# Kernel optimization log

Hardware: AMD Instinct MI355X
Metric: run time of the kernel (lower is better)

The kernel has to match this reference:

```python
import jax, jax.numpy as jnp
import numpy as np

N, C, H, W = 8, 256, 28, 28
K = 64
EPS = 1e-12  # F.normalize eps
BN_EPS = 1e-5


def setup_inputs() -> dict:
    key = jax.random.key(0)
    k1, k2, k3 = jax.random.split(key, 3)
    x = jax.random.normal(k1, (N, C, H, W), dtype=jnp.float32)
    conv_w = jax.random.normal(k2, (K, C), dtype=jnp.float32) * 0.05  # 1x1 conv, no bias (vlad_v2=False)
    centroids = jax.random.uniform(k3, (K, C), dtype=jnp.float32)    # torch.rand init
    bn_w = jnp.ones((K * C,), dtype=jnp.float32)
    bn_b = jnp.zeros((K * C,), dtype=jnp.float32)
    return {"x": x, "conv_w": conv_w, "centroids": centroids, "bn_w": bn_w, "bn_b": bn_b}


def _l2norm(v, axis):
    n = jnp.sqrt(jnp.sum(v * v, axis=axis, keepdims=True))
    return v / jnp.maximum(n, EPS)


def reference(x, conv_w, centroids, bn_w, bn_b):
    n, c, h, w = x.shape
    k = centroids.shape[0]
    P = h * w
    # descriptor-wise L2 normalize over channels
    xn = _l2norm(x, axis=1)
    xf = xn.reshape(n, c, P)                                   # (N, C, P)
    # 1x1 conv soft assignment + softmax over clusters
    soft_assign = jnp.einsum('ncp,kc->nkp', xf, conv_w)        # (N, K, P)
    soft_assign = jax.nn.softmax(soft_assign, axis=1)
    # weighted residuals (N, K, C, P)
    residual = (xf[:, None, :, :] - centroids[None, :, :, None]) * soft_assign[:, :, None, :]
    # intra-normalize over flattened (K*C) per spatial location
    rn = jnp.sqrt(jnp.sum(residual * residual, axis=(1, 2), keepdims=True))  # (N,1,1,P)
    residual = residual / jnp.maximum(rn, EPS)
    # sum pool over spatial, then per-cluster L2 normalize over C
    vlad = residual.sum(axis=-1)                               # (N, K, C)
    vlad = _l2norm(vlad, axis=2)
    v = vlad.reshape(n, k * c)
    # BatchNorm1d in training mode: batch stats, biased variance
    mean = jnp.mean(v, axis=0)
    var = jnp.var(v, axis=0)
    v = (v - mean) / jnp.sqrt(var + BN_EPS) * bn_w + bn_b
    # final L2 normalize
    return _l2norm(v, axis=1)
```

## Files before the change

kernel.cpp:

```cpp
#include <hip/hip_runtime.h>
#include <math.h>

#define N_ 8
#define C_ 256
#define P_ 784
#define K_ 64
#define NP_ 6272
#define F_ 16384
#define FEPS 1e-12f
#define BNEPS 1e-5f

__device__ __forceinline__ float wave_sum(float v) {
#pragma unroll
  for (int s = 1; s < 64; s <<= 1) v += __shfl_xor(v, s, 64);
  return v;
}
__device__ __forceinline__ float wave_max(float v) {
#pragma unroll
  for (int s = 1; s < 64; s <<= 1) v = fmaxf(v, __shfl_xor(v, s, 64));
  return v;
}

__global__ __launch_bounds__(256) void k_prep(const float* __restrict__ x,
                                              const float* __restrict__ cent,
                                              float* __restrict__ rinv,
                                              float* __restrict__ xn2,
                                              float* __restrict__ cn2) {
  __shared__ float red[4][64];
  int b = blockIdx.x, t = threadIdx.x;
  if (b < 25) {
    int tid = b * 256 + t;
    if (tid < NP_) {
      int n = tid / P_, p = tid % P_;
      const float* base = x + (size_t)n * C_ * P_ + p;
      float ssq = 0.f;
#pragma unroll 8
      for (int c = 0; c < C_; ++c) { float v = base[(size_t)c * P_]; ssq += v * v; }
      float r = 1.0f / fmaxf(sqrtf(ssq), FEPS);
      rinv[tid] = r;
      xn2[tid] = ssq * r * r;
    }
  } else {
    int k = t & 63, part = t >> 6;
    const float* row = cent + (size_t)k * C_ + part * 64;
    float s = 0.f;
#pragma unroll 8
    for (int i = 0; i < 64; ++i) { float v = row[i]; s += v * v; }
    red[part][k] = s;
    __syncthreads();
    if (t < 64) cn2[t] = red[0][t] + red[1][t] + red[2][t] + red[3][t];
  }
}

__global__ __launch_bounds__(256) void k_gemm1(const float* __restrict__ x,
                                               const float* __restrict__ convw,
                                               const float* __restrict__ cent,
                                               float* __restrict__ Gp) {
  __shared__ float AsT[32][68];
  __shared__ float Xs[32][68];
  int z = blockIdx.z;
  int n = z >> 1, half = z & 1;
  int kk0 = blockIdx.y * 64;
  int p0 = blockIdx.x * 64;
  int t = threadIdx.x;
  int tx = t & 15, ty = t >> 4;
  float acc[4][4] = {};
  const float* xb = x + (size_t)n * C_ * P_;
  int cbase = half * 128;
  for (int c0 = cbase; c0 < cbase + 128; c0 += 32) {
    {
      int r = t >> 5, cc = t & 31;
#pragma unroll
      for (int i = 0; i < 8; ++i) {
        int row = r + i * 8;
        int kk = kk0 + row;
        const float* Ar = (kk < 64) ? (convw + (size_t)kk * C_) : (cent + (size_t)(kk - 64) * C_);
        AsT[cc][row] = Ar[c0 + cc];
      }
    }
    {
      int rr = t >> 6, pp = t & 63;
#pragma unroll
      for (int i = 0; i < 8; ++i) {
        int c = rr + i * 4;
        int p = p0 + pp;
        Xs[c][pp] = (p < P_) ? xb[(size_t)(c0 + c) * P_ + p] : 0.f;
      }
    }
    __syncthreads();
#pragma unroll
    for (int cc = 0; cc < 32; ++cc) {
      float4 a = *(const float4*)&AsT[cc][ty * 4];
      float4 bv = *(const float4*)&Xs[cc][tx * 4];
      float av[4] = {a.x, a.y, a.z, a.w};
      float bb[4] = {bv.x, bv.y, bv.z, bv.w};
#pragma unroll
      for (int i = 0; i < 4; ++i)
#pragma unroll
        for (int j = 0; j < 4; ++j) acc[i][j] += av[i] * bb[j];
    }
    __syncthreads();
  }
  float* Gb = Gp + (size_t)(half * N_ + n) * P_ * 128;
#pragma unroll
  for (int j = 0; j < 4; ++j) {
    int p = p0 + tx * 4 + j;
    if (p < P_) {
      float4 v = make_float4(acc[0][j], acc[1][j], acc[2][j], acc[3][j]);
      *(float4*)&Gb[(size_t)p * 128 + kk0 + ty * 4] = v;
    }
  }
}

__global__ __launch_bounds__(256) void k_assign(const float* __restrict__ Gp,
                                                const float* __restrict__ rinv,
                                                const float* __restrict__ xn2v,
                                                const float* __restrict__ cn2,
                                                float* __restrict__ w2,
                                                float* __restrict__ Spart) {
  __shared__ float w2_lds[64][17];
  __shared__ float w_lds[64][17];
  int n = blockIdx.y;
  int p0 = blockIdx.x * 16;
  int t = threadIdx.x;
  int wv = t >> 6, lane = t & 63;
  float c2 = cn2[lane];
  const float* Gb0 = Gp + (size_t)n * P_ * 128;
  const float* Gb1 = Gp + (size_t)(N_ + n) * P_ * 128;
  for (int j = 0; j < 4; ++j) {
    int p = p0 + wv * 4 + j;
    float r = rinv[n * P_ + p];
    float lg = (Gb0[(size_t)p * 128 + lane] + Gb1[(size_t)p * 128 + lane]) * r;
    float dt = (Gb0[(size_t)p * 128 + 64 + lane] + Gb1[(size_t)p * 128 + 64 + lane]) * r;
    float m = wave_max(lg);
    float e = expf(lg - m);
    float ssum = wave_sum(e);
    float a = e / ssum;
    float x2 = xn2v[n * P_ + p];
    float rn2 = wave_sum(a * a * (x2 - 2.f * dt + c2));
    float wf = 1.0f / fmaxf(sqrtf(rn2), FEPS);
    float wval = a * wf;
    w_lds[lane][wv * 4 + j] = wval;
    w2_lds[lane][wv * 4 + j] = wval * r;
  }
  __syncthreads();
  {
    int pp = t & 15, k4 = t >> 4;
    float* wb = w2 + (size_t)n * K_ * P_ + p0 + pp;
#pragma unroll
    for (int i = 0; i < 4; ++i) {
      int k = k4 + i * 16;
      wb[(size_t)k * P_] = w2_lds[k][pp];
    }
  }
  if (t < 64) {
    float s = 0.f;
#pragma unroll
    for (int pp = 0; pp < 16; ++pp) s += w_lds[t][pp];
    Spart[((size_t)blockIdx.x * N_ + n) * 64 + t] = s;
  }
}

__global__ __launch_bounds__(256) void k_gemm2(const float* __restrict__ x,
                                               const float* __restrict__ w2,
                                               float* __restrict__ vpart) {
  __shared__ float WsT[32][68];
  __shared__ float XsT[32][68];
  int n = blockIdx.z, s = blockIdx.y;
  int c0 = blockIdx.x * 64;
  int t = threadIdx.x;
  int tx = t & 15, ty = t >> 4;
  float acc[4][4] = {};
  const float* wb = w2 + (size_t)n * K_ * P_;
  const float* xb = x + (size_t)n * C_ * P_;
  int pbase = s * 98;
  for (int q = 0; q < 98; q += 32) {
    int r = t >> 5, pc = t & 31;
    bool ok = (q + pc) < 98;
    int p = pbase + q + pc;
#pragma unroll
    for (int i = 0; i < 8; ++i) {
      int row = r + i * 8;
      WsT[pc][row] = ok ? wb[(size_t)row * P_ + p] : 0.f;
      XsT[pc][row] = ok ? xb[(size_t)(c0 + row) * P_ + p] : 0.f;
    }
    __syncthreads();
#pragma unroll
    for (int pp = 0; pp < 32; ++pp) {
      float4 a = *(const float4*)&WsT[pp][ty * 4];
      float4 bv = *(const float4*)&XsT[pp][tx * 4];
      float av[4] = {a.x, a.y, a.z, a.w};
      float bb[4] = {bv.x, bv.y, bv.z, bv.w};
#pragma unroll
      for (int i = 0; i < 4; ++i)
#pragma unroll
        for (int j = 0; j < 4; ++j) acc[i][j] += av[i] * bb[j];
    }
    __syncthreads();
  }
  float* vb = vpart + (size_t)(s * N_ + n) * K_ * C_;
#pragma unroll
  for (int i = 0; i < 4; ++i)
#pragma unroll
    for (int j = 0; j < 4; ++j)
      vb[(size_t)(ty * 4 + i) * C_ + c0 + tx * 4 + j] = acc[i][j];
}

__global__ __launch_bounds__(256) void k_vladnorm(const float* __restrict__ vpart,
                                                  const float* __restrict__ cent,
                                                  const float* __restrict__ Spart,
                                                  float* __restrict__ vladn) {
  __shared__ float red[4];
  int b = blockIdx.x;
  int n = b >> 6, k = b & 63;
  int c = threadIdx.x;
  float Sb = 0.f;
#pragma unroll
  for (int s = 0; s < 49; ++s) Sb += Spart[((size_t)s * N_ + n) * 64 + k];
  float val = 0.f;
#pragma unroll
  for (int s = 0; s < 8; ++s) val += vpart[(size_t)(s * 512 + b) * C_ + c];
  val -= cent[(size_t)k * C_ + c] * Sb;
  float ss = wave_sum(val * val);
  int wv = threadIdx.x >> 6, lane = threadIdx.x & 63;
  if (lane == 0) red[wv] = ss;
  __syncthreads();
  float tot = red[0] + red[1] + red[2] + red[3];
  float inv = 1.0f / fmaxf(sqrtf(tot), FEPS);
  vladn[(size_t)b * C_ + c] = val * inv;
}

__global__ __launch_bounds__(256) void k_bn(const float* __restrict__ vladn,
                                            const float* __restrict__ bnw,
                                            const float* __restrict__ bnb,
                                            float* __restrict__ ybuf,
                                            float* __restrict__ nrmpart) {
  __shared__ float red[4][8];
  int f = blockIdx.x * 256 + threadIdx.x;
  float v[N_];
  float s = 0.f;
#pragma unroll
  for (int n = 0; n < N_; ++n) { v[n] = vladn[(size_t)n * F_ + f]; s += v[n]; }
  float mean = s * (1.0f / N_);
  float s2 = 0.f;
#pragma unroll
  for (int n = 0; n < N_; ++n) { float d = v[n] - mean; s2 += d * d; }
  float var = s2 * (1.0f / N_);
  float sc = bnw[f] / sqrtf(var + BNEPS);
  float bb = bnb[f];
  float y[N_];
#pragma unroll
  for (int n = 0; n < N_; ++n) {
    y[n] = (v[n] - mean) * sc + bb;
    ybuf[(size_t)n * F_ + f] = y[n];
  }
  int wv = threadIdx.x >> 6, lane = threadIdx.x & 63;
#pragma unroll
  for (int n = 0; n < N_; ++n) {
    float q = wave_sum(y[n] * y[n]);
    if (lane == 0) red[wv][n] = q;
  }
  __syncthreads();
  if (threadIdx.x < N_) {
    int n = threadIdx.x;
    nrmpart[n * 64 + blockIdx.x] = red[0][n] + red[1][n] + red[2][n] + red[3][n];
  }
}

__global__ __launch_bounds__(256) void k_final(const float* __restrict__ ybuf,
                                               const float* __restrict__ nrmpart,
                                               float* __restrict__ out) {
  int idx = blockIdx.x * 256 + threadIdx.x;
  int n = idx >> 14;
  float tot = 0.f;
#pragma unroll
  for (int b = 0; b < 64; ++b) tot += nrmpart[n * 64 + b];
  float inv = 1.0f / fmaxf(sqrtf(tot), FEPS);
  out[idx] = ybuf[idx] * inv;
}

extern "C" void kernel_launch(void* const* d_in, const int* in_sizes, int n_in,
                              void* d_out, int out_size, void* d_ws, size_t ws_size,
                              hipStream_t stream) {
  const float* x = (const float*)d_in[0];
  const float* convw = (const float*)d_in[1];
  const float* cent = (const float*)d_in[2];
  const float* bnw = (const float*)d_in[3];
  const float* bnb = (const float*)d_in[4];
  float* out = (float*)d_out;
  float* ws = (float*)d_ws;

  float* rinv = ws;
  float* xn2 = ws + 6272;
  float* cn2 = ws + 12544;
  float* Spart = ws + 12608;
  float* nrmpart = ws + 37696;
  float* Gp = ws + 38208;
  float* w2 = ws + 1643840;
  float* vpart = ws + 2045248;
  float* vladn = ws + 3093824;
  float* ybuf = ws + 3224896;

  k_prep<<<26, 256, 0, stream>>>(x, cent, rinv, xn2, cn2);
  k_gemm1<<<dim3(13, 2, 16), 256, 0, stream>>>(x, convw, cent, Gp);
  k_assign<<<dim3(49, 8), 256, 0, stream>>>(Gp, rinv, xn2, cn2, w2, Spart);
  k_gemm2<<<dim3(4, 8, 8), 256, 0, stream>>>(x, w2, vpart);
  k_vladnorm<<<512, 256, 0, stream>>>(vpart, cent, Spart, vladn);
  k_bn<<<64, 256, 0, stream>>>(vladn, bnw, bnb, ybuf, nrmpart);
  k_final<<<512, 256, 0, stream>>>(ybuf, nrmpart, out);
}
```

Before: 68.26 us.

## Fuse prep, assignment GEMM and softmax assign into a single kernel

Replaces the separate k_prep, k_gemm1 and k_assign kernels with one k_fused1 kernel. Each block owns 32 spatial positions of one image. It computes the full-channel logits and centroid dot products, the descriptor norms and the centroid norms in LDS, then does softmax and intra-normalization in place. This removes two kernel launches and the global round trip of the split-K GEMM partials. The cost is fewer blocks (200) with less parallel work per launch, and the Spart partial count drops from 49 to 25.

```diff
diff --git a/kernel.cpp b/kernel.cpp
--- a/kernel.cpp
+++ b/kernel.cpp
@@ -5,10 +5,10 @@
 #define C_ 256
 #define P_ 784
 #define K_ 64
-#define NP_ 6272
 #define F_ 16384
 #define FEPS 1e-12f
 #define BNEPS 1e-5f
+#define PBLK 25
 
 __device__ __forceinline__ float wave_sum(float v) {
 #pragma unroll
@@ -21,143 +21,137 @@
   return v;
 }
 
-__global__ __launch_bounds__(256) void k_prep(const float* __restrict__ x,
-                                              const float* __restrict__ cent,
-                                              float* __restrict__ rinv,
-                                              float* __restrict__ xn2,
-                                              float* __restrict__ cn2) {
-  __shared__ float red[4][64];
-  int b = blockIdx.x, t = threadIdx.x;
-  if (b < 25) {
-    int tid = b * 256 + t;
-    if (tid < NP_) {
-      int n = tid / P_, p = tid % P_;
-      const float* base = x + (size_t)n * C_ * P_ + p;
-      float ssq = 0.f;
-#pragma unroll 8
-      for (int c = 0; c < C_; ++c) { float v = base[(size_t)c * P_]; ssq += v * v; }
-      float r = 1.0f / fmaxf(sqrtf(ssq), FEPS);
-      rinv[tid] = r;
-      xn2[tid] = ssq * r * r;
-    }
-  } else {
-    int k = t & 63, part = t >> 6;
-    const float* row = cent + (size_t)k * C_ + part * 64;
-    float s = 0.f;
-#pragma unroll 8
-    for (int i = 0; i < 64; ++i) { float v = row[i]; s += v * v; }
-    red[part][k] = s;
-    __syncthreads();
-    if (t < 64) cn2[t] = red[0][t] + red[1][t] + red[2][t] + red[3][t];
-  }
-}
-
-__global__ __launch_bounds__(256) void k_gemm1(const float* __restrict__ x,
-                                               const float* __restrict__ convw,
-                                               const float* __restrict__ cent,
-                                               float* __restrict__ Gp) {
-  __shared__ float AsT[32][68];
-  __shared__ float Xs[32][68];
-  int z = blockIdx.z;
-  int n = z >> 1, half = z & 1;
-  int kk0 = blockIdx.y * 64;
-  int p0 = blockIdx.x * 64;
-  int t = threadIdx.x;
-  int tx = t & 15, ty = t >> 4;
-  float acc[4][4] = {};
-  const float* xb = x + (size_t)n * C_ * P_;
-  int cbase = half * 128;
-  for (int c0 = cbase; c0 < cbase + 128; c0 += 32) {
-    {
-      int r = t >> 5, cc = t & 31;
-#pragma unroll
-      for (int i = 0; i < 8; ++i) {
-        int row = r + i * 8;
-        int kk = kk0 + row;
-        const float* Ar = (kk < 64) ? (convw + (size_t)kk * C_) : (cent + (size_t)(kk - 64) * C_);
-        AsT[cc][row] = Ar[c0 + cc];
-      }
-    }
-    {
-      int rr = t >> 6, pp = t & 63;
-#pragma unroll
-      for (int i = 0; i < 8; ++i) {
-        int c = rr + i * 4;
-        int p = p0 + pp;
-        Xs[c][pp] = (p < P_) ? xb[(size_t)(c0 + c) * P_ + p] : 0.f;
-      }
-    }
-    __syncthreads();
-#pragma unroll
-    for (int cc = 0; cc < 32; ++cc) {
-      float4 a = *(const float4*)&AsT[cc][ty * 4];
-      float4 bv = *(const float4*)&Xs[cc][tx * 4];
-      float av[4] = {a.x, a.y, a.z, a.w};
-      float bb[4] = {bv.x, bv.y, bv.z, bv.w};
-#pragma unroll
-      for (int i = 0; i < 4; ++i)
-#pragma unroll
-        for (int j = 0; j < 4; ++j) acc[i][j] += av[i] * bb[j];
-    }
-    __syncthreads();
-  }
-  float* Gb = Gp + (size_t)(half * N_ + n) * P_ * 128;
-#pragma unroll
-  for (int j = 0; j < 4; ++j) {
-    int p = p0 + tx * 4 + j;
-    if (p < P_) {
-      float4 v = make_float4(acc[0][j], acc[1][j], acc[2][j], acc[3][j]);
-      *(float4*)&Gb[(size_t)p * 128 + kk0 + ty * 4] = v;
-    }
-  }
-}
-
-__global__ __launch_bounds__(256) void k_assign(const float* __restrict__ Gp,
-                                                const float* __restrict__ rinv,
-                                                const float* __restrict__ xn2v,
-                                                const float* __restrict__ cn2,
+__global__ __launch_bounds__(256) void k_fused1(const float* __restrict__ x,
+                                                const float* __restrict__ convw,
+                                                const float* __restrict__ cent,
                                                 float* __restrict__ w2,
                                                 float* __restrict__ Spart) {
-  __shared__ float w2_lds[64][17];
-  __shared__ float w_lds[64][17];
-  int n = blockIdx.y;
-  int p0 = blockIdx.x * 16;
+  __shared__ float As[128][33];
+  __shared__ float Xs[32][36];
+  __shared__ float G_lds[128][33];
+  __shared__ float w2_lds[64][33];
+  __shared__ float ssq_lds[8][32];
+  __shared__ float cn2p[256];
+  __shared__ float cn2_lds[64];
+  __shared__ float rinv_lds[32];
+  __shared__ float xn2_lds[32];
+  __shared__ float sp_lds[4][64];
+
+  int pblk = blockIdx.x, n = blockIdx.y;
+  int p0 = pblk * 32;
   int t = threadIdx.x;
   int wv = t >> 6, lane = t & 63;
-  float c2 = cn2[lane];
-  const float* Gb0 = Gp + (size_t)n * P_ * 128;
-  const float* Gb1 = Gp + (size_t)(N_ + n) * P_ * 128;
-  for (int j = 0; j < 4; ++j) {
-    int p = p0 + wv * 4 + j;
-    float r = rinv[n * P_ + p];
-    float lg = (Gb0[(size_t)p * 128 + lane] + Gb1[(size_t)p * 128 + lane]) * r;
-    float dt = (Gb0[(size_t)p * 128 + 64 + lane] + Gb1[(size_t)p * 128 + 64 + lane]) * r;
+  const float* xb = x + (size_t)n * C_ * P_;
+
+  {
+    int k = t >> 2, q = t & 3;
+    const float* row = cent + (size_t)k * C_ + q * 64;
+    float s = 0.f;
+#pragma unroll
+    for (int i = 0; i < 16; ++i) {
+      float4 v = *(const float4*)&row[i * 4];
+      s += v.x * v.x + v.y * v.y + v.z * v.z + v.w * v.w;
+    }
+    cn2p[t] = s;
+  }
+
+  int ty = t >> 3, tx = t & 7;
+  float acc[4][4] = {};
+  float ssq_reg = 0.f;
+
+  for (int ch = 0; ch < 8; ++ch) {
+    int c0 = ch * 32;
+    {
+      int cc = t & 31, kg = t >> 5;
+#pragma unroll
+      for (int i = 0; i < 16; ++i) {
+        int kk = kg * 16 + i;
+        const float* Ar = (kk < 64) ? (convw + (size_t)kk * C_) : (cent + (size_t)(kk - 64) * C_);
+        As[kk][cc] = Ar[c0 + cc];
+      }
+    }
+    {
+      int pp = t & 31, cg = t >> 5;
+      int p = p0 + pp;
+      bool ok = p < P_;
+#pragma unroll
+      for (int i = 0; i < 4; ++i) {
+        int cl = cg * 4 + i;
+        float v = ok ? xb[(size_t)(c0 + cl) * P_ + p] : 0.f;
+        Xs[cl][pp] = v;
+        ssq_reg += v * v;
+      }
+    }
+    __syncthreads();
+    if (ch == 0 && t < 64)
+      cn2_lds[t] = cn2p[t * 4] + cn2p[t * 4 + 1] + cn2p[t * 4 + 2] + cn2p[t * 4 + 3];
+#pragma unroll
+    for (int cc = 0; cc < 32; ++cc) {
+      float4 xv = *(const float4*)&Xs[cc][tx * 4];
+      float xa[4] = {xv.x, xv.y, xv.z, xv.w};
+#pragma unroll
+      for (int i = 0; i < 4; ++i) {
+        float a = As[ty * 4 + i][cc];
+#pragma unroll
+        for (int j = 0; j < 4; ++j) acc[i][j] += a * xa[j];
+      }
+    }
+    __syncthreads();
+  }
+
+#pragma unroll
+  for (int i = 0; i < 4; ++i)
+#pragma unroll
+    for (int j = 0; j < 4; ++j) G_lds[ty * 4 + i][tx * 4 + j] = acc[i][j];
+  ssq_lds[t >> 5][t & 31] = ssq_reg;
+  __syncthreads();
+  if (t < 32) {
+    float s = 0.f;
+#pragma unroll
+    for (int g = 0; g < 8; ++g) s += ssq_lds[g][t];
+    float r = 1.0f / fmaxf(sqrtf(s), FEPS);
+    rinv_lds[t] = r;
+    xn2_lds[t] = s * r * r;
+  }
+  __syncthreads();
+
+  float s_acc = 0.f;
+  float c2 = cn2_lds[lane];
+  for (int jp = 0; jp < 8; ++jp) {
+    int pl = wv * 8 + jp;
+    if (p0 + pl >= P_) break;
+    float r = rinv_lds[pl];
+    float x2 = xn2_lds[pl];
+    float lg = G_lds[lane][pl] * r;
+    float dt = G_lds[64 + lane][pl] * r;
     float m = wave_max(lg);
     float e = expf(lg - m);
     float ssum = wave_sum(e);
     float a = e / ssum;
-    float x2 = xn2v[n * P_ + p];
     float rn2 = wave_sum(a * a * (x2 - 2.f * dt + c2));
     float wf = 1.0f / fmaxf(sqrtf(rn2), FEPS);
     float wval = a * wf;
-    w_lds[lane][wv * 4 + j] = wval;
-    w2_lds[lane][wv * 4 + j] = wval * r;
-  }
-  __syncthreads();
+    s_acc += wval;
+    w2_lds[lane][pl] = wval * r;
+  }
+  sp_lds[wv][lane] = s_acc;
+  __syncthreads();
+  if (t < 64) {
+    float s = sp_lds[0][t] + sp_lds[1][t] + sp_lds[2][t] + sp_lds[3][t];
+    Spart[((size_t)pblk * N_ + n) * 64 + t] = s;
+  }
   {
-    int pp = t & 15, k4 = t >> 4;
-    float* wb = w2 + (size_t)n * K_ * P_ + p0 + pp;
-#pragma unroll
-    for (int i = 0; i < 4; ++i) {
-      int k = k4 + i * 16;
-      wb[(size_t)k * P_] = w2_lds[k][pp];
-    }
-  }
-  if (t < 64) {
-    float s = 0.f;
-#pragma unroll
-    for (int pp = 0; pp < 16; ++pp) s += w_lds[t][pp];
-    Spart[((size_t)blockIdx.x * N_ + n) * 64 + t] = s;
+    int q = t & 7;
+#pragma unroll
+    for (int it = 0; it < 2; ++it) {
+      int k = (t >> 3) + 32 * it;
+      int pidx = q * 4;
+      if (p0 + pidx + 3 < P_) {
+        float4 v = make_float4(w2_lds[k][pidx], w2_lds[k][pidx + 1],
+                               w2_lds[k][pidx + 2], w2_lds[k][pidx + 3]);
+        *(float4*)&w2[((size_t)n * K_ + k) * P_ + p0 + pidx] = v;
+      }
+    }
   }
 }
 
@@ -216,7 +210,7 @@
   int c = threadIdx.x;
   float Sb = 0.f;
 #pragma unroll
-  for (int s = 0; s < 49; ++s) Sb += Spart[((size_t)s * N_ + n) * 64 + k];
+  for (int s = 0; s < PBLK; ++s) Sb += Spart[((size_t)s * N_ + n) * 64 + k];
   float val = 0.f;
 #pragma unroll
   for (int s = 0; s < 8; ++s) val += vpart[(size_t)(s * 512 + b) * C_ + c];
@@ -290,20 +284,14 @@
   float* out = (float*)d_out;
   float* ws = (float*)d_ws;
 
-  float* rinv = ws;
-  float* xn2 = ws + 6272;
-  float* cn2 = ws + 12544;
-  float* Spart = ws + 12608;
-  float* nrmpart = ws + 37696;
-  float* Gp = ws + 38208;
-  float* w2 = ws + 1643840;
-  float* vpart = ws + 2045248;
-  float* vladn = ws + 3093824;
-  float* ybuf = ws + 3224896;
-
-  k_prep<<<26, 256, 0, stream>>>(x, cent, rinv, xn2, cn2);
-  k_gemm1<<<dim3(13, 2, 16), 256, 0, stream>>>(x, convw, cent, Gp);
-  k_assign<<<dim3(49, 8), 256, 0, stream>>>(Gp, rinv, xn2, cn2, w2, Spart);
+  float* Spart = ws;
+  float* nrmpart = ws + 12800;
+  float* w2 = ws + 13312;
+  float* vpart = ws + 414720;
+  float* vladn = ws + 1463296;
+  float* ybuf = ws + 1594368;
+
+  k_fused1<<<dim3(PBLK, N_), 256, 0, stream>>>(x, convw, cent, w2, Spart);
   k_gemm2<<<dim3(4, 8, 8), 256, 0, stream>>>(x, w2, vpart);
   k_vladnorm<<<512, 256, 0, stream>>>(vpart, cent, Spart, vladn);
   k_bn<<<64, 256, 0, stream>>>(vladn, bnw, bnb, ybuf, nrmpart);
```

Measured after the change: 62.13 us. 9.0% less time.
